# Kernel optimization log

Hardware: AMD Instinct MI355X
Metric: run time of the kernel (lower is better)

## Reference

```python
import jax, jax.numpy as jnp
import numpy as np

K = 16          # kNN neighbors
CURVE_LEN = 4   # walk length
B, N = 4, 8192


def setup_inputs() -> dict:
    key = jax.random.key(0)
    k1, k2 = jax.random.split(key)
    xyz = jax.random.normal(k1, (B, N, 3), dtype=jnp.float32)
    # torch.randint(1, k, (B, N)) for each of curve_len-1 steps
    rand_k = jax.random.randint(k2, (CURVE_LEN - 1, B, N), 1, K, dtype=jnp.int32)
    return {"xyz": xyz, "rand_k": rand_k}


def reference(xyz, rand_k):
    Bb, Nn, _ = xyz.shape
    # Squared pairwise distances (monotone in true distance -> same top-k order as cdist)
    sq = jnp.sum(xyz * xyz, axis=-1)                                   # (B, N)
    d2 = sq[:, :, None] + sq[:, None, :] - 2.0 * jnp.einsum(
        'bnd,bmd->bnm', xyz, xyz)                                      # (B, N, N)
    # k smallest distances -> negate and take top_k
    _, knn_idx = jax.lax.top_k(-d2, K)                                 # (B, N, K)

    init = jnp.broadcast_to(jnp.arange(Nn, dtype=jnp.int32), (Bb, Nn))  # (B, N)

    def step(cur, rk):
        # rows[b, n, :] = knn_idx[b, cur[b, n], :]
        rows = jnp.take_along_axis(knn_idx, cur[:, :, None], axis=1)   # (B, N, K)
        nxt = jnp.take_along_axis(rows, rk[:, :, None], axis=2)[..., 0]  # (B, N)
        return nxt, nxt

    _, steps = jax.lax.scan(step, init, rand_k)                         # (L-1, B, N)
    curves = jnp.concatenate([init[None], steps], axis=0)               # (L, B, N)
    return jnp.moveaxis(curves, 0, -1)                                  # (B, N, L)
```

## Files before the change

### kernel.cpp

```cpp
#include <hip/hip_runtime.h>
#include <stdint.h>

#define KNN 16
#define CLEN 4
#define NB 4
#define NP 8192
#define G 16
#define NC (G * G * G)
#define GLO -4.5f
#define INVW 1.7777777777777777f
#define CSPLIT 8
#define CHUNK (NP / CSPLIT)
#define QPB 64
#define TPB (QPB * CSPLIT)
#define SDEPTH 12
#define TWIN 128


__device__ __forceinline__ unsigned sp3(unsigned v) {
  v = (v | (v << 16)) & 0x030000FFu;
  v = (v | (v << 8)) & 0x0300F00Fu;
  v = (v | (v << 4)) & 0x030C30C3u;
  v = (v | (v << 2)) & 0x09249249u;
  return v;
}
__device__ __forceinline__ int morton3(int cx, int cy, int cz) {
  return (int)(sp3((unsigned)cx) | (sp3((unsigned)cy) << 1) | (sp3((unsigned)cz) << 2));
}
__device__ __forceinline__ int cell1(float v) {
  int c = (int)floorf((v - GLO) * INVW);
  return min(G - 1, max(0, c));
}

__global__ void bin_kernel(const float* __restrict__ xyz, int* __restrict__ cellid,
                           int* __restrict__ hist) {
  int t = blockIdx.x * blockDim.x + threadIdx.x;
  if (t >= NB * NP) return;
  int b = t >> 13;
  int m = morton3(cell1(xyz[t * 3 + 0]), cell1(xyz[t * 3 + 1]), cell1(xyz[t * 3 + 2]));
  cellid[t] = m;
  atomicAdd(&hist[b * NC + m], 1);
}

__global__ __launch_bounds__(1024) void scan_kernel(const int* __restrict__ hist,
                                                    int* __restrict__ offs) {
  __shared__ int s[1024];
  int b = blockIdx.x, t = threadIdx.x;
  int base = b * NC + t * 4;
  int v0 = hist[base + 0], v1 = hist[base + 1], v2 = hist[base + 2], v3 = hist[base + 3];
  int sum = v0 + v1 + v2 + v3;
  s[t] = sum;
  __syncthreads();
  for (int d = 1; d < 1024; d <<= 1) {
    int x = 0;
    if (t >= d) x = s[t - d];
    __syncthreads();
    if (t >= d) s[t] += x;
    __syncthreads();
  }
  int run = s[t] - sum;
  offs[base + 0] = run; run += v0;
  offs[base + 1] = run; run += v1;
  offs[base + 2] = run; run += v2;
  offs[base + 3] = run;
}

__global__ void scatter_kernel(const float* __restrict__ xyz, const int* __restrict__ cellid,
                               const int* __restrict__ offs, int* __restrict__ cursor,
                               float4* __restrict__ scand, int* __restrict__ sidx,
                               float4* __restrict__ cand) {
#pragma clang fp contract(off)
  int t = blockIdx.x * blockDim.x + threadIdx.x;
  if (t >= NB * NP) return;
  int b = t >> 13, n = t & (NP - 1);
  float x = xyz[t * 3 + 0], y = xyz[t * 3 + 1], z = xyz[t * 3 + 2];
  float sq = (x * x + y * y) + z * z;
  cand[t] = make_float4(x, y, z, sq);
  int m = cellid[t];
  int pos = offs[b * NC + m] + atomicAdd(&cursor[b * NC + m], 1);
  scand[b * NP + pos] = make_float4(x, y, z, sq);
  sidx[b * NP + pos] = n;
}

__global__ void thresh_kernel(const float4* __restrict__ scand, const int* __restrict__ sidx,
                              float* __restrict__ thr) {
#pragma clang fp contract(off)
  int s = blockIdx.x * blockDim.x + threadIdx.x;
  if (s >= NB * NP) return;
  int b = s >> 13;
  int bbase = b * NP;
  float4 qd = scand[s];
  int w0 = s - (TWIN / 2);
  if (w0 < bbase) w0 = bbase;
  if (w0 > bbase + NP - TWIN) w0 = bbase + NP - TWIN;
  float dist[KNN];
#pragma unroll
  for (int j = 0; j < KNN; ++j) dist[j] = __builtin_inff();
#pragma unroll 1
  for (int i = 0; i < TWIN; i += 8) {
    float4 c0 = scand[w0 + i + 0];
    float4 c1 = scand[w0 + i + 1];
    float4 c2 = scand[w0 + i + 2];
    float4 c3 = scand[w0 + i + 3];
    float4 c4 = scand[w0 + i + 4];
    float4 c5 = scand[w0 + i + 5];
    float4 c6 = scand[w0 + i + 6];
    float4 c7 = scand[w0 + i + 7];
#define TPROC(cc)                                                   \
    do {                                                            \
      float p0 = qd.x * (cc).x;                                     \
      float dot = fmaf(qd.z, (cc).z, fmaf(qd.y, (cc).y, p0));       \
      float d2 = fmaf(-2.0f, dot, qd.w + (cc).w);                   \
      _Pragma("unroll")                                             \
      for (int j = KNN - 1; j >= 1; --j)                            \
        dist[j] = __builtin_amdgcn_fmed3f(dist[j - 1], dist[j], d2);\
      dist[0] = fminf(dist[0], d2);                                 \
    } while (0)
    TPROC(c0); TPROC(c1); TPROC(c2); TPROC(c3);
    TPROC(c4); TPROC(c5); TPROC(c6); TPROC(c7);
#undef TPROC
  }
  thr[bbase + sidx[s]] = dist[KNN - 1];
}

#define INSERT(dv, iv)                                              \
  do {                                                              \
    float _d = (dv); int _i = (iv);                                 \
    bool c[KNN];                                                    \
    _Pragma("unroll")                                               \
    for (int j = 0; j < KNN; ++j) c[j] = dist[j] > _d;              \
    _Pragma("unroll")                                               \
    for (int j = KNN - 1; j >= 1; --j) {                            \
      dist[j] = __builtin_amdgcn_fmed3f(dist[j - 1], dist[j], _d);  \
      idx[j] = c[j - 1] ? idx[j - 1] : (c[j] ? _i : idx[j]);        \
    }                                                               \
    dist[0] = fminf(dist[0], _d);                                   \
    idx[0] = c[0] ? _i : idx[0];                                    \
  } while (0)

#define FLUSH()                                                \
  do {                                                         \
    int pc = (int)(sp - spbase) / TPB;                         \
    float2 e[SDEPTH];                                          \
    _Pragma("unroll")                                          \
    for (int j = 0; j < SDEPTH; ++j) e[j] = stk[j * TPB + t];  \
    _Pragma("unroll")                                          \
    for (int j = 0; j < SDEPTH; ++j) {                         \
      if (!__any(j < pc)) break;                               \
      bool act = j < pc;                                       \
      float fd = act ? e[j].x : __builtin_inff();              \
      int fi = __float_as_int(e[j].y);                         \
      INSERT(fd, fi);                                          \
    }                                                          \
    sp = spbase;                                               \
    dmax = fminf(dmax, dist[KNN - 1]);                         \
    hb = (qd.w - dmax) * 0.5f - 5e-4f;                         \
  } while (0)

__global__ __launch_bounds__(TPB, 4) void knn_kernel(const float4* __restrict__ cand,
                                                     const float* __restrict__ thr,
                                                     int* __restrict__ knn) {
#pragma clang fp contract(off)
  __shared__ __align__(16) char smem[65536];
  float2* stk = (float2*)smem;

  const int t = threadIdx.x;
  const int lane = t & 63;
  const int wid = t >> 6;
  const int bq = blockIdx.x * QPB + lane;
  const int b = bq >> 13;
  const float4 qd = cand[bq];
  const float4* cb = cand + b * NP;

  float dist[KNN];
  int idx[KNN];
#pragma unroll
  for (int j = 0; j < KNN; ++j) { dist[j] = __builtin_inff(); idx[j] = 0; }
  float dmax = thr[bq];
  float hb = (qd.w - dmax) * 0.5f - 5e-4f;

  float2* const spbase = stk + t;
  float2* const slim = stk + t + (SDEPTH - 7) * TPB;
  float2* sp = spbase;

  const int m0 = wid * CHUNK;
  float4* sb = ((float4*)(smem + 49152)) + (size_t)wid * 128;

  float4 r = cb[m0 + lane];
  sb[lane] = r;
  r = cb[m0 + 64 + lane];
  int p = 0;

#pragma unroll 1
  for (int s = 0; s < CHUNK; s += 64) {
    asm volatile("s_waitcnt lgkmcnt(0)" ::: "memory");
    if (s + 64 < CHUNK) {
      sb[(p ^ 1) * 64 + lane] = r;
      if (s + 128 < CHUNK) r = cb[m0 + s + 128 + lane];
    }
    const float4* cur = sb + p * 64;
#pragma unroll 1
    for (int g = 0; g < 64; g += 8) {
      float4 c0 = cur[g + 0];
      float4 c1 = cur[g + 1];
      float4 c2 = cur[g + 2];
      float4 c3 = cur[g + 3];
      float4 c4 = cur[g + 4];
      float4 c5 = cur[g + 5];
      float4 c6 = cur[g + 6];
      float4 c7 = cur[g + 7];
#define PROC(cc, mm)                                                \
      do {                                                          \
        float p0 = qd.x * (cc).x;                                   \
        float dot = fmaf(qd.z, (cc).z, fmaf(qd.y, (cc).y, p0));     \
        float hc = fmaf(0.5f, (cc).w, hb);                          \
        if (dot >= hc) {           \
          float d2 = fmaf(-2.0f, dot, qd.w + (cc).w);    \
          *sp = make_float2(d2, __int_as_float(mm));                \
          sp += TPB;                                                \
        }                                                           \
      } while (0)
      PROC(c0, m0 + s + g + 0);
      PROC(c1, m0 + s + g + 1);
      PROC(c2, m0 + s + g + 2);
      PROC(c3, m0 + s + g + 3);
      PROC(c4, m0 + s + g + 4);
      PROC(c5, m0 + s + g + 5);
      PROC(c6, m0 + s + g + 6);
      PROC(c7, m0 + s + g + 7);
#undef PROC
      if (__any(sp >= slim)) FLUSH();
    }
    p ^= 1;
  }
  FLUSH();

  __syncthreads();
  float2* tl = (float2*)smem;
  float2* al = (float2*)(smem + 32768);

  if (wid < 4) {
#pragma unroll
    for (int j = 0; j < KNN; ++j)
      tl[j * (4 * QPB) + t] = make_float2(dist[j], __int_as_float(idx[j]));
  }
  __syncthreads();
  if (t < QPB) {
    int p4[4] = {0, 0, 0, 0};
#pragma unroll 1
    for (int j = 0; j < KNN; ++j) {
      float bd = __builtin_inff();
      int bi = 0, bc = 0;
#pragma unroll
      for (int c = 0; c < 4; ++c) {
        bool v = p4[c] < KNN;
        int pp = v ? p4[c] : 0;
        float2 e = tl[pp * (4 * QPB) + t + c * QPB];
        float hd = v ? e.x : __builtin_inff();
        if (hd < bd || c == 0) { bd = hd; bi = __float_as_int(e.y); bc = c; }
      }
      al[j * QPB + t] = make_float2(bd, __int_as_float(bi));
#pragma unroll
      for (int c = 0; c < 4; ++c) p4[c] += (bc == c);
    }
  }
  __syncthreads();

  if (wid >= 4) {
#pragma unroll
    for (int j = 0; j < KNN; ++j)
      tl[j * (4 * QPB) + (t - 4 * QPB)] = make_float2(dist[j], __int_as_float(idx[j]));
  }
  __syncthreads();
  if (t < QPB) {
    int p5[5] = {0, 0, 0, 0, 0};
    int* kn = knn + bq * KNN;
#pragma unroll 1
    for (int j = 0; j < KNN; ++j) {
      float bd;
      int bi, bc;
      {
        bool v = p5[0] < KNN;
        int pp = v ? p5[0] : 0;
        float2 e = al[pp * QPB + t];
        bd = v ? e.x : __builtin_inff();
        bi = __float_as_int(e.y);
        bc = 0;
      }
#pragma unroll
      for (int c = 0; c < 4; ++c) {
        bool v = p5[c + 1] < KNN;
        int pp = v ? p5[c + 1] : 0;
        float2 e = tl[pp * (4 * QPB) + t + c * QPB];
        float hd = v ? e.x : __builtin_inff();
        if (hd < bd) { bd = hd; bi = __float_as_int(e.y); bc = c + 1; }
      }
      kn[j] = bi;
#pragma unroll
      for (int c = 0; c < 5; ++c) p5[c] += (bc == c);
    }
  }
}

__global__ void walk_kernel(const int* __restrict__ rand_k, const int* __restrict__ knn,
                            int* __restrict__ out) {
  int t = blockIdx.x * blockDim.x + threadIdx.x;
  if (t >= NB * NP) return;
  int b = t >> 13;
  int n = t & (NP - 1);
  int cur = n;
  int* o = out + t * CLEN;
  o[0] = cur;
#pragma unroll
  for (int l = 0; l < CLEN - 1; ++l) {
    int rk = rand_k[(l * NB + b) * NP + n];
    cur = knn[(b * NP + cur) * KNN + rk];
    o[l + 1] = cur;
  }
}

extern "C" void kernel_launch(void* const* d_in, const int* in_sizes, int n_in,
                              void* d_out, int out_size, void* d_ws, size_t ws_size,
                              hipStream_t stream) {
  const float* xyz = (const float*)d_in[0];
  const int* rand_k = (const int*)d_in[1];
  int* out = (int*)d_out;

  char* w = (char*)d_ws;
  float4* cand  = (float4*)(w);
  float4* scand = (float4*)(w + 524288);
  int* sidx     = (int*)(w + 1048576);
  float* thr    = (float*)(w + 1179648);
  int* knnt     = (int*)(w + 1310720);
  int* cellid   = (int*)(w + 3407872);
  int* hist     = (int*)(w + 3538944);
  int* cursor   = (int*)(w + 3604480);
  int* offs     = (int*)(w + 3670016);

  hipMemsetAsync(hist, 0, 131072, stream);

  bin_kernel<<<(NB * NP + 255) / 256, 256, 0, stream>>>(xyz, cellid, hist);
  scan_kernel<<<NB, 1024, 0, stream>>>(hist, offs);
  scatter_kernel<<<(NB * NP + 255) / 256, 256, 0, stream>>>(xyz, cellid, offs, cursor,
                                                            scand, sidx, cand);
  thresh_kernel<<<(NB * NP + 255) / 256, 256, 0, stream>>>(scand, sidx, thr);
  knn_kernel<<<(NB * NP) / QPB, TPB, 0, stream>>>(cand, thr, knnt);
  walk_kernel<<<(NB * NP + 255) / 256, 256, 0, stream>>>(rand_k, knnt, out);
}
```

Before: 120.4 us.

## Split candidate scan across 16 chunks with 32 queries per block

Each block now takes 32 queries and splits the candidate set into 16 chunks instead of 64 queries over 8 chunks. Each wavefront therefore covers two chunks, one per 32-lane half. The per-thread spill stack is made shallower and flushed twice per group of eight candidates, and shared memory drops to 48KB. The final merge goes from 4/5-way to 8/9-way to match the extra chunks. The aim is more blocks and more parallelism, and possibly better occupancy. The cost is a longer serial merge on 32 threads and more frequent flushes.

```diff
diff --git a/kernel.cpp b/kernel.cpp
--- a/kernel.cpp
+++ b/kernel.cpp
@@ -9,11 +9,11 @@
 #define NC (G * G * G)
 #define GLO -4.5f
 #define INVW 1.7777777777777777f
-#define CSPLIT 8
+#define CSPLIT 16
 #define CHUNK (NP / CSPLIT)
-#define QPB 64
+#define QPB 32
 #define TPB (QPB * CSPLIT)
-#define SDEPTH 12
+#define SDEPTH 8
 #define TWIN 128
 
 
@@ -161,13 +161,13 @@
                                                      const float* __restrict__ thr,
                                                      int* __restrict__ knn) {
 #pragma clang fp contract(off)
-  __shared__ __align__(16) char smem[65536];
+  __shared__ __align__(16) char smem[49152];
   float2* stk = (float2*)smem;
 
   const int t = threadIdx.x;
-  const int lane = t & 63;
-  const int wid = t >> 6;
-  const int bq = blockIdx.x * QPB + lane;
+  const int q_local = t & (QPB - 1);
+  const int chunk = t >> 5;
+  const int bq = blockIdx.x * QPB + q_local;
   const int b = bq >> 13;
   const float4 qd = cand[bq];
   const float4* cb = cand + b * NP;
@@ -180,27 +180,28 @@
   float hb = (qd.w - dmax) * 0.5f - 5e-4f;
 
   float2* const spbase = stk + t;
-  float2* const slim = stk + t + (SDEPTH - 7) * TPB;
+  float2* const slim = stk + t + (SDEPTH - 4) * TPB;
   float2* sp = spbase;
 
-  const int m0 = wid * CHUNK;
-  float4* sb = ((float4*)(smem + 49152)) + (size_t)wid * 128;
-
-  float4 r = cb[m0 + lane];
-  sb[lane] = r;
-  r = cb[m0 + 64 + lane];
+  const int m0 = chunk * CHUNK;
+  const int hl = q_local;
+  float4* sb = ((float4*)(smem + 32768)) + (size_t)chunk * 64;
+
+  float4 r = cb[m0 + hl];
+  sb[hl] = r;
+  r = cb[m0 + 32 + hl];
   int p = 0;
 
 #pragma unroll 1
-  for (int s = 0; s < CHUNK; s += 64) {
+  for (int s = 0; s < CHUNK; s += 32) {
     asm volatile("s_waitcnt lgkmcnt(0)" ::: "memory");
-    if (s + 64 < CHUNK) {
-      sb[(p ^ 1) * 64 + lane] = r;
-      if (s + 128 < CHUNK) r = cb[m0 + s + 128 + lane];
+    if (s + 32 < CHUNK) {
+      sb[(p ^ 1) * 32 + hl] = r;
+      if (s + 64 < CHUNK) r = cb[m0 + s + 64 + hl];
     }
-    const float4* cur = sb + p * 64;
-#pragma unroll 1
-    for (int g = 0; g < 64; g += 8) {
+    const float4* cur = sb + p * 32;
+#pragma unroll 1
+    for (int g = 0; g < 32; g += 8) {
       float4 c0 = cur[g + 0];
       float4 c1 = cur[g + 1];
       float4 c2 = cur[g + 2];
@@ -224,12 +225,13 @@
       PROC(c1, m0 + s + g + 1);
       PROC(c2, m0 + s + g + 2);
       PROC(c3, m0 + s + g + 3);
+      if (__any(sp >= slim)) FLUSH();
       PROC(c4, m0 + s + g + 4);
       PROC(c5, m0 + s + g + 5);
       PROC(c6, m0 + s + g + 6);
       PROC(c7, m0 + s + g + 7);
+      if (__any(sp >= slim)) FLUSH();
 #undef PROC
-      if (__any(sp >= slim)) FLUSH();
     }
     p ^= 1;
   }
@@ -239,65 +241,69 @@
   float2* tl = (float2*)smem;
   float2* al = (float2*)(smem + 32768);
 
-  if (wid < 4) {
+  if (chunk < 8) {
 #pragma unroll
     for (int j = 0; j < KNN; ++j)
-      tl[j * (4 * QPB) + t] = make_float2(dist[j], __int_as_float(idx[j]));
+      tl[j * (8 * QPB) + t] = make_float2(dist[j], __int_as_float(idx[j]));
   }
   __syncthreads();
   if (t < QPB) {
-    int p4[4] = {0, 0, 0, 0};
+    int p8[8];
+#pragma unroll
+    for (int c = 0; c < 8; ++c) p8[c] = 0;
 #pragma unroll 1
     for (int j = 0; j < KNN; ++j) {
       float bd = __builtin_inff();
       int bi = 0, bc = 0;
 #pragma unroll
-      for (int c = 0; c < 4; ++c) {
-        bool v = p4[c] < KNN;
-        int pp = v ? p4[c] : 0;
-        float2 e = tl[pp * (4 * QPB) + t + c * QPB];
+      for (int c = 0; c < 8; ++c) {
+        bool v = p8[c] < KNN;
+        int pp = v ? p8[c] : 0;
+        float2 e = tl[pp * (8 * QPB) + t + c * QPB];
         float hd = v ? e.x : __builtin_inff();
         if (hd < bd || c == 0) { bd = hd; bi = __float_as_int(e.y); bc = c; }
       }
       al[j * QPB + t] = make_float2(bd, __int_as_float(bi));
 #pragma unroll
-      for (int c = 0; c < 4; ++c) p4[c] += (bc == c);
+      for (int c = 0; c < 8; ++c) p8[c] += (bc == c);
     }
   }
   __syncthreads();
 
-  if (wid >= 4) {
+  if (chunk >= 8) {
 #pragma unroll
     for (int j = 0; j < KNN; ++j)
-      tl[j * (4 * QPB) + (t - 4 * QPB)] = make_float2(dist[j], __int_as_float(idx[j]));
+      tl[j * (8 * QPB) + (t - 8 * QPB)] = make_float2(dist[j], __int_as_float(idx[j]));
   }
   __syncthreads();
   if (t < QPB) {
-    int p5[5] = {0, 0, 0, 0, 0};
+    int p9[9];
+#pragma unroll
+    for (int c = 0; c < 9; ++c) p9[c] = 0;
     int* kn = knn + bq * KNN;
 #pragma unroll 1
     for (int j = 0; j < KNN; ++j) {
       float bd;
       int bi, bc;
       {
-        bool v = p5[0] < KNN;
-        int pp = v ? p5[0] : 0;
+        bool v = p9[0] < KNN;
+        int pp = v ? p9[0] : 0;
         float2 e = al[pp * QPB + t];
         bd = v ? e.x : __builtin_inff();
         bi = __float_as_int(e.y);
         bc = 0;
       }
 #pragma unroll
-      for (int c = 0; c < 4; ++c) {
-        bool v = p5[c + 1] < KNN;
-        int pp = v ? p5[c + 1] : 0;
-        float2 e = tl[pp * (4 * QPB) + t + c * QPB];
+      for (int c = 0; c < 8; ++c) {
+        bool v = p9[c + 1] < KNN;
+        int pp = v ? p9[c + 1] : 0;
+        float2 e = tl[pp * (8 * QPB) + t + c * QPB];
         float hd = v ? e.x : __builtin_inff();
         if (hd < bd) { bd = hd; bi = __float_as_int(e.y); bc = c + 1; }
       }
       kn[j] = bi;
 #pragma unroll
-      for (int c = 0; c < 5; ++c) p5[c] += (bc == c);
+      for (int c = 0; c < 9; ++c) p9[c] += (bc == c);
     }
   }
 }
```

After: 148.9 us. 23.7% more time.
